# Optimization experiments

Measured on AMD Instinct MI355X. Metric: run time of the kernel, lower is better.

## Reference

```python
import jax, jax.numpy as jnp
import numpy as np

B, S, D, FF, V, H, M = 4, 512, 768, 3072, 30000, 12, 64
DH = D // H
N_LAYERS = 12  # shared ALBERT layer applied 12 times


def _positional_encoding():
    pos = jnp.arange(S, dtype=jnp.float32)[:, None]                      # [S,1]
    denom = jnp.power(10000.0, 2.0 * jnp.arange(D, dtype=jnp.float32) / D)
    pe = pos / denom                                                     # [S,D]
    pe = pe.at[1:, 0::2].set(jnp.sin(pe[1:, 0::2]))
    pe = pe.at[1:, 1::2].set(jnp.cos(pe[1:, 1::2]))
    return pe


def setup_inputs() -> dict:
    key = jax.random.key(0)
    ks = jax.random.split(key, 20)
    tok = jax.random.randint(ks[0], (B, S), 0, V)
    texts_onehot = jax.nn.one_hot(tok, V, dtype=jnp.float32)
    w = lambda k, shp: (jax.random.normal(k, shp, jnp.float32) * 0.02)
    return {
        'texts_onehot': texts_onehot,
        'se_w': w(ks[1], (V, D)), 'se_b': w(ks[2], (D,)),
        'wq': w(ks[3], (D, D)), 'bq': w(ks[4], (D,)),
        'wk': w(ks[5], (D, D)), 'bk': w(ks[6], (D,)),
        'wv': w(ks[7], (D, D)), 'bv': w(ks[8], (D,)),
        'wo': w(ks[9], (D, D)), 'bo': w(ks[10], (D,)),
        'w1': w(ks[11], (D, FF)), 'b1': w(ks[12], (FF,)),
        'w2': w(ks[13], (FF, D)), 'b2': w(ks[14], (D,)),
        'we': w(ks[15], (D, V)), 'be': w(ks[16], (V,)),
        'idx': jax.random.randint(ks[17], (B, M), 0, S),
    }


def _layernorm(x):
    mean = jnp.mean(x, axis=-1, keepdims=True)
    var = jnp.mean(jnp.square(x - mean), axis=-1, keepdims=True)
    return (x - mean) / jnp.sqrt(var + 1e-5)


def reference(texts_onehot, se_w, se_b, wq, bq, wk, bk, wv, bv, wo, bo,
              w1, b1, w2, b2, we, be, idx):
    pe = _positional_encoding()                                          # [S,D]
    x = texts_onehot @ se_w + se_b + pe                                  # [B,S,D]
    scale = 1.0 / jnp.sqrt(jnp.float32(DH))

    def mha(x):
        q = (x @ wq + bq).reshape(B, S, H, DH)
        k = (x @ wk + bk).reshape(B, S, H, DH)
        v = (x @ wv + bv).reshape(B, S, H, DH)
        att = jax.nn.softmax(jnp.einsum('bqhd,bkhd->bhqk', q, k) * scale, axis=-1)
        o = jnp.einsum('bhqk,bkhd->bqhd', att, v).reshape(B, S, D)
        return o @ wo + bo

    for _ in range(N_LAYERS):  # same (shared) weights every iteration
        x = _layernorm(x + mha(x))
        x = jax.nn.relu(x @ w1 + b1) @ w2 + b2

    # gather masked positions then project to vocab + log_softmax
    g = jnp.take_along_axis(x, idx[..., None], axis=1)                   # [B,M,D]
    logits = g @ we + be                                                 # [B,M,V]
    return jax.nn.log_softmax(logits, axis=-1).reshape(B * M, V)
```

## Files before the change

### kernel.cpp

```cpp
#include <hip/hip_runtime.h>
#include <hip/hip_bf16.h>
#include <math.h>

#define Bv 4
#define Sv 512
#define Dv 768
#define FFv 3072
#define Vv 30000
#define Vpad 30080
#define Hv 12
#define Mv 64
#define DHv 64
#define NLAYERS 12
#define QKVN 2304

typedef __attribute__((ext_vector_type(8))) short short8;
typedef __attribute__((ext_vector_type(4))) float floatx4;

static __device__ __forceinline__ short f2b(float f) {
  union { float f; unsigned u; } v; v.f = f;
  unsigned r = v.u + 0x7fffu + ((v.u >> 16) & 1u);
  return (short)(r >> 16);
}

#define GLD16(gp, lp) __builtin_amdgcn_global_load_lds( \
    (__attribute__((address_space(1))) void*)(gp), \
    (__attribute__((address_space(3))) void*)(lp), 16, 0, 0)

__global__ __launch_bounds__(256) void transpose_w(
    const float* __restrict__ W, short* __restrict__ Wt,
    int K, int N, int Nout)
{
  __shared__ float t[32][33];
  int n0 = blockIdx.x * 32, k0 = blockIdx.y * 32;
  int tx = threadIdx.x & 31, ty = threadIdx.x >> 5;
  #pragma unroll
  for (int i = 0; i < 4; i++) {
    int k = k0 + ty + i * 8, n = n0 + tx;
    t[ty + i * 8][tx] = (n < N) ? W[(size_t)k * N + n] : 0.f;
  }
  __syncthreads();
  #pragma unroll
  for (int i = 0; i < 4; i++) {
    int n = n0 + ty + i * 8, k = k0 + tx;
    if (n < Nout) Wt[(size_t)n * K + k] = f2b(t[tx][ty + i * 8]);
  }
}

__global__ __launch_bounds__(256) void pack_bias(
    const float* __restrict__ bq, const float* __restrict__ bk,
    const float* __restrict__ bv, float* __restrict__ bqkv)
{
  int i = blockIdx.x * 256 + threadIdx.x;
  if (i < Dv) { bqkv[i] = bq[i]; bqkv[Dv + i] = bk[i]; bqkv[2 * Dv + i] = bv[i]; }
}

__global__ __launch_bounds__(256) void embed_kernel(
    const float* __restrict__ oh, const float* __restrict__ sew,
    const float* __restrict__ seb, float* __restrict__ xf,
    short* __restrict__ xb)
{
  int bs = blockIdx.x;
  int s = bs & (Sv - 1);
  __shared__ int tokS;
  const float* row = oh + (size_t)bs * Vv;
  for (int j = threadIdx.x * 4; j < Vv; j += 256 * 4) {
    float4 f = *(const float4*)(row + j);
    if (f.x != 0.f) tokS = j;
    if (f.y != 0.f) tokS = j + 1;
    if (f.z != 0.f) tokS = j + 2;
    if (f.w != 0.f) tokS = j + 3;
  }
  __syncthreads();
  int tok = tokS;
  for (int d = threadIdx.x; d < Dv; d += 256) {
    float pe = 0.f;
    if (s > 0) {
      float denom = expf(9.210340371976184f * (2.f * (float)d / 768.f));
      float raw = (float)s / denom;
      pe = (d & 1) ? cosf(raw) : sinf(raw);
    }
    float val = sew[(size_t)tok * Dv + d] + seb[d] + pe;
    xf[(size_t)bs * Dv + d] = val;
    xb[(size_t)bs * Dv + d] = f2b(val);
  }
}

template <int BM, int BN, int WM, int WN>
__global__ __launch_bounds__(256) void gemm_bt(
    const short* __restrict__ A, const short* __restrict__ Bt,
    const float* __restrict__ bias, float* __restrict__ Cf,
    short* __restrict__ Cb, int M, int N, int K, int relu)
{
  __shared__ __align__(16) short As[BM * 64];
  __shared__ __align__(16) short Bs[BN * 64];
  int n0 = blockIdx.x * BN, m0 = blockIdx.y * BM;
  int tid = threadIdx.x;
  int wave = tid >> 6, lane = tid & 63, quad = lane >> 4, l16 = lane & 15;
  int wm = (wave >> 1) * WM, wn = (wave & 1) * WN;

  floatx4 acc[WM / 16][WN / 16];
  #pragma unroll
  for (int i = 0; i < WM / 16; i++)
    #pragma unroll
    for (int j = 0; j < WN / 16; j++) acc[i][j] = (floatx4){0.f, 0.f, 0.f, 0.f};

  int srow[4], skc[4];
  #pragma unroll
  for (int it = 0; it < 4; it++) {
    int c = it * 256 + tid;
    srow[it] = c >> 3;
    skc[it] = (c & 7) ^ (srow[it] & 7);
  }

  for (int k0 = 0; k0 < K; k0 += 64) {
    __syncthreads();
    #pragma unroll
    for (int it = 0; it < BM / 32; it++)
      GLD16(A + (size_t)(m0 + srow[it]) * K + k0 + skc[it] * 8,
            As + (it * 2048 + wave * 512));
    #pragma unroll
    for (int it = 0; it < BN / 32; it++)
      GLD16(Bt + (size_t)(n0 + srow[it]) * K + k0 + skc[it] * 8,
            Bs + (it * 2048 + wave * 512));
    __syncthreads();
    #pragma unroll
    for (int kh = 0; kh < 2; kh++) {
      short8 af[WM / 16], bfr[WN / 16];
      int kc = kh * 4 + quad;
      #pragma unroll
      for (int i = 0; i < WM / 16; i++) {
        int ra = wm + i * 16 + l16;
        af[i] = *(const short8*)(As + (ra * 8 + (kc ^ (ra & 7))) * 8);
      }
      #pragma unroll
      for (int j = 0; j < WN / 16; j++) {
        int rb = wn + j * 16 + l16;
        bfr[j] = *(const short8*)(Bs + (rb * 8 + (kc ^ (rb & 7))) * 8);
      }
      #pragma unroll
      for (int i = 0; i < WM / 16; i++)
        #pragma unroll
        for (int j = 0; j < WN / 16; j++)
          acc[i][j] = __builtin_amdgcn_mfma_f32_16x16x32_bf16(af[i], bfr[j], acc[i][j], 0, 0, 0);
    }
  }

  #pragma unroll
  for (int i = 0; i < WM / 16; i++) {
    int row = m0 + wm + i * 16 + quad * 4;
    #pragma unroll
    for (int j = 0; j < WN / 16; j++) {
      int col = n0 + wn + j * 16 + l16;
      if (col < N) {
        float bb = bias ? bias[col] : 0.f;
        #pragma unroll
        for (int r = 0; r < 4; r++) {
          float val = acc[i][j][r] + bb;
          if (relu) val = fmaxf(val, 0.f);
          size_t off = (size_t)(row + r) * N + col;
          if (Cf) Cf[off] = val;
          if (Cb) Cb[off] = f2b(val);
        }
      }
    }
  }
}

__global__ __launch_bounds__(256) void attn_fused(
    const short* __restrict__ qkv, short* __restrict__ O)
{
  __shared__ __align__(16) short lv[64][40];
  __shared__ __align__(16) short pbuf[4][16][40];
  int q0 = blockIdx.x * 64;
  int bh = blockIdx.y;
  int b = bh / Hv, h = bh - b * Hv;
  int tid = threadIdx.x;
  int wave = tid >> 6, lane = tid & 63, quad = lane >> 4, l16 = lane & 15;

  floatx4 acc[32];
  #pragma unroll
  for (int c = 0; c < 32; c++) acc[c] = (floatx4){0.f, 0.f, 0.f, 0.f};

  const short* Qrow = qkv + (size_t)(b * Sv + q0 + wave * 16 + l16) * QKVN + h * DHv;
  short8 a0 = *(const short8*)(Qrow + quad * 8);
  short8 a1 = *(const short8*)(Qrow + 32 + quad * 8);
  const short* Kbase = qkv + Dv + (size_t)(b * Sv + l16) * QKVN + h * DHv + quad * 8;
  #pragma unroll
  for (int c = 0; c < 32; c++) {
    const short* Kp = Kbase + (size_t)c * 16 * QKVN;
    short8 b0 = *(const short8*)(Kp);
    short8 b1 = *(const short8*)(Kp + 32);
    acc[c] = __builtin_amdgcn_mfma_f32_16x16x32_bf16(a0, b0, acc[c], 0, 0, 0);
    acc[c] = __builtin_amdgcn_mfma_f32_16x16x32_bf16(a1, b1, acc[c], 0, 0, 0);
  }

  float inv[4];
  #pragma unroll
  for (int r = 0; r < 4; r++) {
    float m = -1e30f;
    #pragma unroll
    for (int c = 0; c < 32; c++) m = fmaxf(m, acc[c][r]);
    m = fmaxf(m, __shfl_xor(m, 1));
    m = fmaxf(m, __shfl_xor(m, 2));
    m = fmaxf(m, __shfl_xor(m, 4));
    m = fmaxf(m, __shfl_xor(m, 8));
    float s = 0.f;
    #pragma unroll
    for (int c = 0; c < 32; c++) {
      float e = __expf((acc[c][r] - m) * 0.125f);
      acc[c][r] = e; s += e;
    }
    s += __shfl_xor(s, 1);
    s += __shfl_xor(s, 2);
    s += __shfl_xor(s, 4);
    s += __shfl_xor(s, 8);
    inv[r] = 1.f / s;
  }

  floatx4 acc_o[4];
  #pragma unroll
  for (int j = 0; j < 4; j++) acc_o[j] = (floatx4){0.f, 0.f, 0.f, 0.f};

  const short* Vbase = qkv + 2 * Dv + h * DHv + (size_t)(b * Sv) * QKVN;
  for (int kc = 0; kc < 16; kc++) {
    __syncthreads();
    #pragma unroll
    for (int i = 0; i < 4; i++) {
      int u = i * 256 + tid;
      int kk = u >> 5, nn2 = (u & 31) * 2;
      const short* vp = Vbase + (size_t)(kc * 32 + kk) * QKVN + nn2;
      short v0 = vp[0], v1 = vp[1];
      lv[nn2][kk] = v0;
      lv[nn2 + 1][kk] = v1;
    }
    #pragma unroll
    for (int half = 0; half < 2; half++) {
      int c = 2 * kc + half;
      #pragma unroll
      for (int r = 0; r < 4; r++)
        pbuf[wave][quad * 4 + r][half * 16 + l16] = f2b(acc[c][r] * inv[r]);
    }
    __syncthreads();
    short8 af = *(const short8*)(&pbuf[wave][l16][quad * 8]);
    #pragma unroll
    for (int j = 0; j < 4; j++) {
      short8 bf = *(const short8*)(&lv[j * 16 + l16][quad * 8]);
      acc_o[j] = __builtin_amdgcn_mfma_f32_16x16x32_bf16(af, bf, acc_o[j], 0, 0, 0);
    }
  }

  int row = q0 + wave * 16 + quad * 4;
  #pragma unroll
  for (int j = 0; j < 4; j++) {
    int col = h * DHv + j * 16 + l16;
    #pragma unroll
    for (int r = 0; r < 4; r++)
      O[(size_t)(b * Sv + row + r) * Dv + col] = f2b(acc_o[j][r]);
  }
}

__global__ __launch_bounds__(256) void addln_kernel(
    float* __restrict__ xf, const float* __restrict__ mh,
    short* __restrict__ xb)
{
  int r = blockIdx.x, t = threadIdx.x;
  size_t base = (size_t)r * Dv;
  float v[3];
  #pragma unroll
  for (int i = 0; i < 3; i++) {
    int d = t + i * 256;
    v[i] = xf[base + d] + mh[base + d];
  }
  __shared__ float red[256];
  red[t] = v[0] + v[1] + v[2];
  __syncthreads();
  for (int s2 = 128; s2 > 0; s2 >>= 1) { if (t < s2) red[t] += red[t + s2]; __syncthreads(); }
  float mean = red[0] * (1.f / 768.f);
  __syncthreads();
  float sq = 0.f;
  #pragma unroll
  for (int i = 0; i < 3; i++) { float d2 = v[i] - mean; sq += d2 * d2; }
  red[t] = sq;
  __syncthreads();
  for (int s2 = 128; s2 > 0; s2 >>= 1) { if (t < s2) red[t] += red[t + s2]; __syncthreads(); }
  float inv = rsqrtf(red[0] * (1.f / 768.f) + 1e-5f);
  #pragma unroll
  for (int i = 0; i < 3; i++) {
    int d = t + i * 256;
    float o = (v[i] - mean) * inv;
    xf[base + d] = o;
    xb[base + d] = f2b(o);
  }
}

__global__ __launch_bounds__(256) void gather_kernel(
    const short* __restrict__ xb, const int* __restrict__ idx,
    short* __restrict__ g)
{
  int bm = blockIdx.x;
  int b = bm >> 6;
  int s = idx[bm];
  for (int d = threadIdx.x; d < Dv; d += 256)
    g[(size_t)bm * Dv + d] = xb[(size_t)(b * Sv + s) * Dv + d];
}

__global__ __launch_bounds__(256) void lsm_kernel(
    const float* __restrict__ L, float* __restrict__ out)
{
  int r = blockIdx.x, t = threadIdx.x;
  const float* p = L + (size_t)r * Vv;
  float m = -1e30f;
  for (int j = t; j < Vv; j += 256) m = fmaxf(m, p[j]);
  __shared__ float red[256];
  red[t] = m;
  __syncthreads();
  for (int s2 = 128; s2 > 0; s2 >>= 1) { if (t < s2) red[t] = fmaxf(red[t], red[t + s2]); __syncthreads(); }
  m = red[0];
  __syncthreads();
  float s = 0.f;
  for (int j = t; j < Vv; j += 256) s += expf(p[j] - m);
  red[t] = s;
  __syncthreads();
  for (int s2 = 128; s2 > 0; s2 >>= 1) { if (t < s2) red[t] += red[t + s2]; __syncthreads(); }
  float lse = m + logf(red[0]);
  for (int j = t; j < Vv; j += 256) out[(size_t)r * Vv + j] = p[j] - lse;
}

extern "C" void kernel_launch(void* const* d_in, const int* in_sizes, int n_in,
                              void* d_out, int out_size, void* d_ws, size_t ws_size,
                              hipStream_t stream) {
  const float* oh  = (const float*)d_in[0];
  const float* sew = (const float*)d_in[1];
  const float* seb = (const float*)d_in[2];
  const float* wq  = (const float*)d_in[3];  const float* bq = (const float*)d_in[4];
  const float* wk  = (const float*)d_in[5];  const float* bk = (const float*)d_in[6];
  const float* wv  = (const float*)d_in[7];  const float* bv = (const float*)d_in[8];
  const float* wo  = (const float*)d_in[9];  const float* bo = (const float*)d_in[10];
  const float* w1  = (const float*)d_in[11]; const float* b1 = (const float*)d_in[12];
  const float* w2  = (const float*)d_in[13]; const float* b2 = (const float*)d_in[14];
  const float* we  = (const float*)d_in[15]; const float* be = (const float*)d_in[16];
  const int*   idx = (const int*)d_in[17];
  float* out = (float*)d_out;

  char* p = (char*)d_ws;
  auto alloc = [&](size_t bytes) -> char* {
    char* r = p; p += (bytes + 255) & ~(size_t)255; return r;
  };
  const size_t BS = (size_t)Bv * Sv;
  short* wqkv_t = (short*)alloc((size_t)QKVN * Dv * 2);
  short* wo_t   = (short*)alloc((size_t)Dv * Dv * 2);
  short* w1_t   = (short*)alloc((size_t)FFv * Dv * 2);
  short* w2_t   = (short*)alloc((size_t)Dv * FFv * 2);
  float* bqkv   = (float*)alloc(QKVN * 4);
  short* xb     = (short*)alloc(BS * Dv * 2);
  float* xf     = (float*)alloc(BS * Dv * 4);
  short* g      = (short*)alloc((size_t)Bv * Mv * Dv * 2);
  char*  TR     = p;
  short* qkv   = (short*)TR;
  short* o     = (short*)(TR + ((BS * QKVN * 2 + 255) & ~(size_t)255));
  float* mh    = (float*)((char*)o + ((BS * Dv * 2 + 255) & ~(size_t)255));
  short* t1    = (short*)((char*)mh + ((BS * Dv * 4 + 255) & ~(size_t)255));
  short* we_t = (short*)TR;
  float* lg   = (float*)(TR + (((size_t)Vpad * Dv * 2 + 255) & ~(size_t)255));

  transpose_w<<<dim3(24, 24), 256, 0, stream>>>(wq, wqkv_t,            Dv, Dv, Dv);
  transpose_w<<<dim3(24, 24), 256, 0, stream>>>(wk, wqkv_t + Dv * Dv,  Dv, Dv, Dv);
  transpose_w<<<dim3(24, 24), 256, 0, stream>>>(wv, wqkv_t + 2*Dv*Dv,  Dv, Dv, Dv);
  transpose_w<<<dim3(24, 24), 256, 0, stream>>>(wo, wo_t,              Dv, Dv, Dv);
  transpose_w<<<dim3(96, 24), 256, 0, stream>>>(w1, w1_t,              Dv, FFv, FFv);
  transpose_w<<<dim3(24, 96), 256, 0, stream>>>(w2, w2_t,              FFv, Dv, Dv);
  pack_bias<<<3, 256, 0, stream>>>(bq, bk, bv, bqkv);

  embed_kernel<<<(int)BS, 256, 0, stream>>>(oh, sew, seb, xf, xb);

  dim3 gQKV(QKVN / 128, (int)BS / 128);
  dim3 gD64(Dv / 64, (int)BS / 64);
  dim3 gFF(FFv / 128, (int)BS / 128);
  for (int l = 0; l < NLAYERS; l++) {
    gemm_bt<128,128,64,64><<<gQKV, 256, 0, stream>>>(xb, wqkv_t, bqkv, nullptr, qkv, (int)BS, QKVN, Dv, 0);
    attn_fused<<<dim3(Sv / 64, Bv * Hv), 256, 0, stream>>>(qkv, o);
    gemm_bt<64,64,32,32><<<gD64, 256, 0, stream>>>(o, wo_t, bo, mh, nullptr, (int)BS, Dv, Dv, 0);
    addln_kernel<<<(int)BS, 256, 0, stream>>>(xf, mh, xb);
    gemm_bt<128,128,64,64><<<gFF, 256, 0, stream>>>(xb, w1_t, b1, nullptr, t1, (int)BS, FFv, Dv, 1);
    gemm_bt<64,64,32,32><<<gD64, 256, 0, stream>>>(t1, w2_t, b2, xf, xb, (int)BS, Dv, FFv, 0);
  }

  transpose_w<<<dim3(940, 24), 256, 0, stream>>>(we, we_t, Dv, Vv, Vpad);
  gather_kernel<<<Bv * Mv, 256, 0, stream>>>(xb, idx, g);
  gemm_bt<128,128,64,64><<<dim3(Vpad / 128, (Bv * Mv) / 128), 256, 0, stream>>>(
      g, we_t, be, lg, nullptr, Bv * Mv, Vv, Dv, 0);
  lsm_kernel<<<Bv * Mv, 256, 0, stream>>>(lg, out);
}
```

Baseline: 2.424 ms.

## Split-K the output and FFN2 GEMMs, pre-transpose V in the QKV epilogue

The QKV GEMM epilogue now writes V directly in a transposed per-head layout, so attention no longer transposes V through LDS with per-chunk barriers. Attention stores the whole normalized probability matrix in swizzled LDS (64 KB) and reads V fragments straight from global memory. The Wo and W2 GEMMs now use 128x64 tiles with 2-way split-K into fp32 partial buffers. Bias addition and the partial reduction move into addln and a new combine kernel. This trades one extra kernel launch and more partial-sum traffic per layer for more parallelism and fewer synchronisations. The large LDS allocation may reduce attention occupancy.

Result: no change. 2.454 ms (+1.2%).

```diff
diff --git a/kernel.cpp b/kernel.cpp
--- a/kernel.cpp
+++ b/kernel.cpp
@@ -13,6 +13,7 @@
 #define DHv 64
 #define NLAYERS 12
 #define QKVN 2304
+#define MN (2048 * 768)
 
 typedef __attribute__((ext_vector_type(8))) short short8;
 typedef __attribute__((ext_vector_type(4))) float floatx4;
@@ -86,11 +87,12 @@
   }
 }
 
-template <int BM, int BN, int WM, int WN>
+template <int BM, int BN, int WM, int WN, bool WVT>
 __global__ __launch_bounds__(256) void gemm_bt(
     const short* __restrict__ A, const short* __restrict__ Bt,
     const float* __restrict__ bias, float* __restrict__ Cf,
-    short* __restrict__ Cb, int M, int N, int K, int relu)
+    short* __restrict__ Cb, short* __restrict__ vt,
+    int M, int N, int K, int klen, int relu)
 {
   __shared__ __align__(16) short As[BM * 64];
   __shared__ __align__(16) short Bs[BN * 64];
@@ -113,7 +115,8 @@
     skc[it] = (c & 7) ^ (srow[it] & 7);
   }
 
-  for (int k0 = 0; k0 < K; k0 += 64) {
+  int kbeg = blockIdx.z * klen;
+  for (int k0 = kbeg; k0 < kbeg + klen; k0 += 64) {
     __syncthreads();
     #pragma unroll
     for (int it = 0; it < BM / 32; it++)
@@ -146,6 +149,7 @@
     }
   }
 
+  float* Cfz = Cf ? Cf + (size_t)blockIdx.z * M * N : nullptr;
   #pragma unroll
   for (int i = 0; i < WM / 16; i++) {
     int row = m0 + wm + i * 16 + quad * 4;
@@ -159,8 +163,14 @@
           float val = acc[i][j][r] + bb;
           if (relu) val = fmaxf(val, 0.f);
           size_t off = (size_t)(row + r) * N + col;
-          if (Cf) Cf[off] = val;
-          if (Cb) Cb[off] = f2b(val);
+          if (Cfz) Cfz[off] = val;
+          if (WVT && col >= 1536) {
+            int vc = col - 1536;
+            int vrow = ((row >> 9) * Hv + (vc >> 6)) * 64 + (vc & 63);
+            vt[(size_t)vrow * 512 + (row & 511) + r] = f2b(val);
+          } else if (Cb) {
+            Cb[off] = f2b(val);
+          }
         }
       }
     }
@@ -168,10 +178,10 @@
 }
 
 __global__ __launch_bounds__(256) void attn_fused(
-    const short* __restrict__ qkv, short* __restrict__ O)
-{
-  __shared__ __align__(16) short lv[64][40];
-  __shared__ __align__(16) short pbuf[4][16][40];
+    const short* __restrict__ qkv, const short* __restrict__ vt,
+    short* __restrict__ O)
+{
+  __shared__ __align__(16) short pb[4 * 16 * 512];
   int q0 = blockIdx.x * 64;
   int bh = blockIdx.y;
   int b = bh / Hv, h = bh - b * Hv;
@@ -218,34 +228,27 @@
     inv[r] = 1.f / s;
   }
 
+  short* myp = pb + wave * 8192;
+  #pragma unroll
+  for (int c = 0; c < 32; c++) {
+    int cc = c * 2 + (l16 >> 3);
+    #pragma unroll
+    for (int r = 0; r < 4; r++) {
+      int row = quad * 4 + r;
+      myp[row * 512 + ((cc ^ (row & 7)) << 3) + (l16 & 7)] = f2b(acc[c][r] * inv[r]);
+    }
+  }
+
   floatx4 acc_o[4];
   #pragma unroll
   for (int j = 0; j < 4; j++) acc_o[j] = (floatx4){0.f, 0.f, 0.f, 0.f};
-
-  const short* Vbase = qkv + 2 * Dv + h * DHv + (size_t)(b * Sv) * QKVN;
-  for (int kc = 0; kc < 16; kc++) {
-    __syncthreads();
-    #pragma unroll
-    for (int i = 0; i < 4; i++) {
-      int u = i * 256 + tid;
-      int kk = u >> 5, nn2 = (u & 31) * 2;
-      const short* vp = Vbase + (size_t)(kc * 32 + kk) * QKVN + nn2;
-      short v0 = vp[0], v1 = vp[1];
-      lv[nn2][kk] = v0;
-      lv[nn2 + 1][kk] = v1;
-    }
-    #pragma unroll
-    for (int half = 0; half < 2; half++) {
-      int c = 2 * kc + half;
-      #pragma unroll
-      for (int r = 0; r < 4; r++)
-        pbuf[wave][quad * 4 + r][half * 16 + l16] = f2b(acc[c][r] * inv[r]);
-    }
-    __syncthreads();
-    short8 af = *(const short8*)(&pbuf[wave][l16][quad * 8]);
+  const short* vbase = vt + (size_t)bh * 64 * 512;
+  for (int kb = 0; kb < 16; kb++) {
+    int cc = kb * 4 + quad;
+    short8 af = *(const short8*)(myp + l16 * 512 + ((cc ^ (l16 & 7)) << 3));
     #pragma unroll
     for (int j = 0; j < 4; j++) {
-      short8 bf = *(const short8*)(&lv[j * 16 + l16][quad * 8]);
+      short8 bf = *(const short8*)(vbase + (size_t)(j * 16 + l16) * 512 + kb * 32 + quad * 8);
       acc_o[j] = __builtin_amdgcn_mfma_f32_16x16x32_bf16(af, bf, acc_o[j], 0, 0, 0);
     }
   }
@@ -261,8 +264,8 @@
 }
 
 __global__ __launch_bounds__(256) void addln_kernel(
-    float* __restrict__ xf, const float* __restrict__ mh,
-    short* __restrict__ xb)
+    float* __restrict__ xf, const float* __restrict__ mhp,
+    const float* __restrict__ bo, short* __restrict__ xb)
 {
   int r = blockIdx.x, t = threadIdx.x;
   size_t base = (size_t)r * Dv;
@@ -270,7 +273,7 @@
   #pragma unroll
   for (int i = 0; i < 3; i++) {
     int d = t + i * 256;
-    v[i] = xf[base + d] + mh[base + d];
+    v[i] = xf[base + d] + mhp[base + d] + mhp[MN + base + d] + bo[d];
   }
   __shared__ float red[256];
   red[t] = v[0] + v[1] + v[2];
@@ -291,6 +294,21 @@
     float o = (v[i] - mean) * inv;
     xf[base + d] = o;
     xb[base + d] = f2b(o);
+  }
+}
+
+__global__ __launch_bounds__(256) void combine2_kernel(
+    const float* __restrict__ p2, const float* __restrict__ b2,
+    float* __restrict__ xf, short* __restrict__ xb)
+{
+  int r = blockIdx.x, t = threadIdx.x;
+  size_t base = (size_t)r * Dv;
+  #pragma unroll
+  for (int i = 0; i < 3; i++) {
+    int d = t + i * 256;
+    float val = p2[base + d] + p2[MN + base + d] + b2[d];
+    xf[base + d] = val;
+    xb[base + d] = f2b(val);
   }
 }
 
@@ -355,12 +373,14 @@
   float* bqkv   = (float*)alloc(QKVN * 4);
   short* xb     = (short*)alloc(BS * Dv * 2);
   float* xf     = (float*)alloc(BS * Dv * 4);
+  short* vt     = (short*)alloc((size_t)Bv * Hv * 64 * 512 * 2);
   short* g      = (short*)alloc((size_t)Bv * Mv * Dv * 2);
   char*  TR     = p;
   short* qkv   = (short*)TR;
   short* o     = (short*)(TR + ((BS * QKVN * 2 + 255) & ~(size_t)255));
-  float* mh    = (float*)((char*)o + ((BS * Dv * 2 + 255) & ~(size_t)255));
-  short* t1    = (short*)((char*)mh + ((BS * Dv * 4 + 255) & ~(size_t)255));
+  float* mhp   = (float*)((char*)o + ((BS * Dv * 2 + 255) & ~(size_t)255));
+  short* t1    = (short*)((char*)mhp + (2 * BS * Dv * 4 + 255 & ~(size_t)255));
+  float* f2p   = (float*)((char*)t1 + ((BS * FFv * 2 + 255) & ~(size_t)255));
   short* we_t = (short*)TR;
   float* lg   = (float*)(TR + (((size_t)Vpad * Dv * 2 + 255) & ~(size_t)255));
 
@@ -375,20 +395,25 @@
   embed_kernel<<<(int)BS, 256, 0, stream>>>(oh, sew, seb, xf, xb);
 
   dim3 gQKV(QKVN / 128, (int)BS / 128);
-  dim3 gD64(Dv / 64, (int)BS / 64);
   dim3 gFF(FFv / 128, (int)BS / 128);
+  dim3 gSK(Dv / 64, (int)BS / 128, 2);
   for (int l = 0; l < NLAYERS; l++) {
-    gemm_bt<128,128,64,64><<<gQKV, 256, 0, stream>>>(xb, wqkv_t, bqkv, nullptr, qkv, (int)BS, QKVN, Dv, 0);
-    attn_fused<<<dim3(Sv / 64, Bv * Hv), 256, 0, stream>>>(qkv, o);
-    gemm_bt<64,64,32,32><<<gD64, 256, 0, stream>>>(o, wo_t, bo, mh, nullptr, (int)BS, Dv, Dv, 0);
-    addln_kernel<<<(int)BS, 256, 0, stream>>>(xf, mh, xb);
-    gemm_bt<128,128,64,64><<<gFF, 256, 0, stream>>>(xb, w1_t, b1, nullptr, t1, (int)BS, FFv, Dv, 1);
-    gemm_bt<64,64,32,32><<<gD64, 256, 0, stream>>>(t1, w2_t, b2, xf, xb, (int)BS, Dv, FFv, 0);
+    gemm_bt<128,128,64,64,true><<<gQKV, 256, 0, stream>>>(
+        xb, wqkv_t, bqkv, nullptr, qkv, vt, (int)BS, QKVN, Dv, Dv, 0);
+    attn_fused<<<dim3(Sv / 64, Bv * Hv), 256, 0, stream>>>(qkv, vt, o);
+    gemm_bt<128,64,64,32,false><<<gSK, 256, 0, stream>>>(
+        o, wo_t, nullptr, mhp, nullptr, nullptr, (int)BS, Dv, Dv, Dv / 2, 0);
+    addln_kernel<<<(int)BS, 256, 0, stream>>>(xf, mhp, bo, xb);
+    gemm_bt<128,128,64,64,false><<<gFF, 256, 0, stream>>>(
+        xb, w1_t, b1, nullptr, t1, nullptr, (int)BS, FFv, Dv, Dv, 1);
+    gemm_bt<128,64,64,32,false><<<gSK, 256, 0, stream>>>(
+        t1, w2_t, nullptr, f2p, nullptr, nullptr, (int)BS, Dv, FFv, FFv / 2, 0);
+    combine2_kernel<<<(int)BS, 256, 0, stream>>>(f2p, b2, xf, xb);
   }
 
   transpose_w<<<dim3(940, 24), 256, 0, stream>>>(we, we_t, Dv, Vv, Vpad);
   gather_kernel<<<Bv * Mv, 256, 0, stream>>>(xb, idx, g);
-  gemm_bt<128,128,64,64><<<dim3(Vpad / 128, (Bv * Mv) / 128), 256, 0, stream>>>(
-      g, we_t, be, lg, nullptr, Bv * Mv, Vv, Dv, 0);
+  gemm_bt<128,128,64,64,false><<<dim3(Vpad / 128, (Bv * Mv) / 128), 256, 0, stream>>>(
+      g, we_t, be, lg, nullptr, nullptr, Bv * Mv, Vv, Dv, Dv, 0);
   lsm_kernel<<<Bv * Mv, 256, 0, stream>>>(lg, out);
 }
```
